# Kernel optimization log

Measured on AMD Instinct MI355X. Metric: run time of the kernel, lower is better.

Reference implementation:

```python
import jax, jax.numpy as jnp
import numpy as np

N_VARS = 4096      # number of discrete variables
CARD = 16          # uniform cardinality per variable
N_HIDDEN = 256
POP = 1024         # pop_size (batch)
N_VISIBLE = N_VARS * CARD  # 65536


def setup_inputs() -> dict:
    key = jax.random.key(0)
    k1, k2, k3 = jax.random.split(key, 3)
    # hidden units are binary stochastic in the RBM; uniform [0,1) works for the math
    hidden = jax.random.uniform(k1, (POP, N_HIDDEN), dtype=jnp.float32)
    W = jax.random.normal(k2, (N_VISIBLE, N_HIDDEN), dtype=jnp.float32) * 0.01
    a = jax.random.normal(k3, (N_VISIBLE,), dtype=jnp.float32) * 0.01
    return {"hidden": hidden, "W": W, "a": a}


def reference(hidden, W, a):
    # prob_visible_given_hidden: activation = hidden @ W^T + a  -> [POP, N_VISIBLE]
    act = jnp.einsum('bh,vh->bv', hidden, W) + a
    # per-variable segmented softmax over each block of CARD visible units
    # (uniform cardinality -> reshape to [POP, N_VARS, CARD] and softmax on last axis)
    prob = jax.nn.softmax(act.reshape(POP, N_VARS, CARD), axis=-1)
    return prob.reshape(POP, N_VISIBLE)
```

## Files before the change

kernel.cpp:

```cpp
#include <hip/hip_runtime.h>
#include <hip/hip_bf16.h>


typedef short  bf16x8 __attribute__((ext_vector_type(8)));
typedef float  f32x4  __attribute__((ext_vector_type(4)));

#define NH    256
#define POP   1024
#define NVIS  65536
#define BM    128
#define BN    128
#define BK    32

__device__ __forceinline__ void gld16(void* lds, const void* g) {
  __builtin_amdgcn_global_load_lds(
      (const __attribute__((address_space(1))) void*)g,
      (__attribute__((address_space(3))) void*)lds,
      16, 0, 0);
}
__device__ __forceinline__ unsigned pack2bf(float lo, float hi) {
  return (__float_as_uint(hi) & 0xffff0000u) | (__float_as_uint(lo) >> 16);
}

__global__ __launch_bounds__(256) void cvt_bf16_kernel(
    const float* __restrict__ src, unsigned short* __restrict__ dst, int n8) {
  int i = blockIdx.x * blockDim.x + threadIdx.x;
  const int stride = gridDim.x * blockDim.x;
  for (; i < n8; i += stride) {
    const float4 f0 = ((const float4*)src)[2 * i];
    const float4 f1 = ((const float4*)src)[2 * i + 1];
    uint4 o;
    o.x = pack2bf(f0.x, f0.y); o.y = pack2bf(f0.z, f0.w);
    o.z = pack2bf(f1.x, f1.y); o.w = pack2bf(f1.z, f1.w);
    ((uint4*)dst)[i] = o;
  }
}

__global__ __launch_bounds__(256) void rbm_gemm_kernel(
    const unsigned short* __restrict__ Wb,
    const unsigned short* __restrict__ Hb,
    const float* __restrict__ Ag,
    float* __restrict__ out)
{
  __shared__ short sA[BM * BK];
  __shared__ short sB[BN * BK];

  const int tid  = threadIdx.x;
  const int lane = tid & 63;
  const int wave = tid >> 6;
  const int wm   = wave & 1;
  const int wn   = wave >> 1;
  const int quad = lane >> 4;
  const int col  = lane & 15;

  const int m_base = blockIdx.y * BM;
  const int n_base = blockIdx.x * BN;

  f32x4 acc[4][4];
  #pragma unroll
  for (int i = 0; i < 4; ++i)
    #pragma unroll
    for (int j = 0; j < 4; ++j)
      acc[i][j] = f32x4{0.f, 0.f, 0.f, 0.f};

  for (int kk = 0; kk < NH / BK; ++kk) {
    const int k0 = kk * BK;
    if (kk) __syncthreads();

    #pragma unroll
    for (int t = 0; t < 2; ++t) {
      const int c   = t * 256 + tid;
      const int row = c >> 2;
      const int cio = (c & 3) * 8;
      gld16(&sA[row * BK + cio], Wb + (size_t)(m_base + row) * NH + k0 + cio);
      gld16(&sB[row * BK + cio], Hb + (size_t)(n_base + row) * NH + k0 + cio);
    }
    __syncthreads();

    bf16x8 af[4], bfr[4];
    #pragma unroll
    for (int mt = 0; mt < 4; ++mt)
      af[mt] = *(const bf16x8*)&sA[(wm * 64 + mt * 16 + col) * BK + quad * 8];
    #pragma unroll
    for (int nt = 0; nt < 4; ++nt)
      bfr[nt] = *(const bf16x8*)&sB[(wn * 64 + nt * 16 + col) * BK + quad * 8];

    #pragma unroll
    for (int mt = 0; mt < 4; ++mt)
      #pragma unroll
      for (int nt = 0; nt < 4; ++nt)
        acc[mt][nt] = __builtin_amdgcn_mfma_f32_16x16x32_bf16(
            af[mt], bfr[nt], acc[mt][nt], 0, 0, 0);
  }

  #pragma unroll
  for (int mt = 0; mt < 4; ++mt) {
    const int v0 = m_base + wm * 64 + mt * 16 + quad * 4;
    const float4 av = *(const float4*)(Ag + v0);
    #pragma unroll
    for (int nt = 0; nt < 4; ++nt) {
      const int b = n_base + wn * 64 + nt * 16 + col;
      f32x4 c = acc[mt][nt];
      float x0 = c[0] + av.x, x1 = c[1] + av.y;
      float x2 = c[2] + av.z, x3 = c[3] + av.w;
      float mx = fmaxf(fmaxf(x0, x1), fmaxf(x2, x3));
      mx = fmaxf(mx, __shfl_xor(mx, 16));
      mx = fmaxf(mx, __shfl_xor(mx, 32));
      float e0 = __expf(x0 - mx), e1 = __expf(x1 - mx);
      float e2 = __expf(x2 - mx), e3 = __expf(x3 - mx);
      float s = (e0 + e1) + (e2 + e3);
      s += __shfl_xor(s, 16);
      s += __shfl_xor(s, 32);
      const float inv = 1.0f / s;
      f32x4 o;
      o[0] = e0 * inv; o[1] = e1 * inv; o[2] = e2 * inv; o[3] = e3 * inv;
      __builtin_nontemporal_store(o, (f32x4*)(out + (size_t)b * NVIS + v0));
    }
  }
}

__global__ __launch_bounds__(256) void rbm_softmax_fb(
    const float* __restrict__ Wg, const float* __restrict__ Hg,
    const float* __restrict__ Ag, float* __restrict__ out)
{
  __shared__ short sA[BM * BK];
  __shared__ short sB[BN * BK];
  const int tid = threadIdx.x, lane = tid & 63, wave = tid >> 6;
  const int wm = wave & 1, wn = wave >> 1, quad = lane >> 4, col = lane & 15;
  const int m_base = blockIdx.y * BM, n_base = blockIdx.x * BN;
  const int r0 = tid >> 3, c0 = (tid & 7) * 4;
  f32x4 acc[4][4];
  #pragma unroll
  for (int i = 0; i < 4; ++i)
    #pragma unroll
    for (int j = 0; j < 4; ++j) acc[i][j] = f32x4{0.f, 0.f, 0.f, 0.f};
  for (int kk = 0; kk < NH / BK; ++kk) {
    const int k0 = kk * BK;
    if (kk) __syncthreads();
    const float* pa = Wg + (size_t)(m_base + r0) * NH + k0 + c0;
    const float* pb = Hg + (size_t)(n_base + r0) * NH + k0 + c0;
    #pragma unroll
    for (int i = 0; i < 4; ++i) {
      const float4 fa = *(const float4*)(pa + (size_t)i * 32 * NH);
      const float4 fb = *(const float4*)(pb + (size_t)i * 32 * NH);
      uint2 ua, ub;
      ua.x = pack2bf(fa.x, fa.y); ua.y = pack2bf(fa.z, fa.w);
      ub.x = pack2bf(fb.x, fb.y); ub.y = pack2bf(fb.z, fb.w);
      *(uint2*)&sA[(i * 32 + r0) * BK + c0] = ua;
      *(uint2*)&sB[(i * 32 + r0) * BK + c0] = ub;
    }
    __syncthreads();
    bf16x8 af[4], bfr[4];
    #pragma unroll
    for (int mt = 0; mt < 4; ++mt)
      af[mt] = *(const bf16x8*)&sA[(wm * 64 + mt * 16 + col) * BK + quad * 8];
    #pragma unroll
    for (int nt = 0; nt < 4; ++nt)
      bfr[nt] = *(const bf16x8*)&sB[(wn * 64 + nt * 16 + col) * BK + quad * 8];
    #pragma unroll
    for (int mt = 0; mt < 4; ++mt)
      #pragma unroll
      for (int nt = 0; nt < 4; ++nt)
        acc[mt][nt] = __builtin_amdgcn_mfma_f32_16x16x32_bf16(
            af[mt], bfr[nt], acc[mt][nt], 0, 0, 0);
  }
  #pragma unroll
  for (int mt = 0; mt < 4; ++mt) {
    const int v0 = m_base + wm * 64 + mt * 16 + quad * 4;
    const float4 av = *(const float4*)(Ag + v0);
    #pragma unroll
    for (int nt = 0; nt < 4; ++nt) {
      const int b = n_base + wn * 64 + nt * 16 + col;
      f32x4 c = acc[mt][nt];
      float x0 = c[0] + av.x, x1 = c[1] + av.y;
      float x2 = c[2] + av.z, x3 = c[3] + av.w;
      float mx = fmaxf(fmaxf(x0, x1), fmaxf(x2, x3));
      mx = fmaxf(mx, __shfl_xor(mx, 16));
      mx = fmaxf(mx, __shfl_xor(mx, 32));
      float e0 = __expf(x0 - mx), e1 = __expf(x1 - mx);
      float e2 = __expf(x2 - mx), e3 = __expf(x3 - mx);
      float s = (e0 + e1) + (e2 + e3);
      s += __shfl_xor(s, 16); s += __shfl_xor(s, 32);
      const float inv = 1.0f / s;
      float4 o;
      o.x = e0 * inv; o.y = e1 * inv; o.z = e2 * inv; o.w = e3 * inv;
      *(float4*)(out + (size_t)b * NVIS + v0) = o;
    }
  }
}

extern "C" void kernel_launch(void* const* d_in, const int* in_sizes, int n_in,
                              void* d_out, int out_size, void* d_ws, size_t ws_size,
                              hipStream_t stream) {
  const float* hidden = (const float*)d_in[0];
  const float* W      = (const float*)d_in[1];
  const float* a      = (const float*)d_in[2];
  float* out          = (float*)d_out;

  const size_t w_elems = (size_t)NVIS * NH;
  const size_t h_elems = (size_t)POP * NH;
  const size_t need = (w_elems + h_elems) * sizeof(unsigned short);

  dim3 grid(POP / BN, NVIS / BM);

  if (ws_size >= need) {
    unsigned short* Wb = (unsigned short*)d_ws;
    unsigned short* Hb = Wb + w_elems;
    cvt_bf16_kernel<<<2048, 256, 0, stream>>>(W, Wb, (int)(w_elems / 8));
    cvt_bf16_kernel<<<128, 256, 0, stream>>>(hidden, Hb, (int)(h_elems / 8));
    rbm_gemm_kernel<<<grid, 256, 0, stream>>>(Wb, Hb, a, out);
  } else {
    rbm_softmax_fb<<<grid, 256, 0, stream>>>(W, hidden, a, out);
  }
}
```

Measured before the change: 394.0 us.

## Fuse bf16 conversion into GEMM, keep hidden tile resident in LDS

Drops the separate fp32-to-bf16 conversion kernels and the workspace round trip. Each block now converts its 128-row hidden tile once into LDS, holding all of K. Each wave streams W rows straight from global memory into registers, converts them in place with a one-step register prefetch, and runs MFMAs against the resident B tile before the fused softmax epilogue. This removes the extra W read/write pass and the per-K-step barriers. In exchange, W fragments are loaded without LDS sharing, and the larger accumulator set (4x8 tiles) raises register pressure under launch bounds of 2 blocks per CU.

```diff
diff --git a/kernel.cpp b/kernel.cpp
--- a/kernel.cpp
+++ b/kernel.cpp
@@ -1,5 +1,4 @@
 #include <hip/hip_runtime.h>
-#include <hip/hip_bf16.h>
 
 
 typedef short  bf16x8 __attribute__((ext_vector_type(8)));
@@ -8,183 +7,128 @@
 #define NH    256
 #define POP   1024
 #define NVIS  65536
-#define BM    128
 #define BN    128
-#define BK    32
+#define MB    1024
+#define SUBM  64
 
-__device__ __forceinline__ void gld16(void* lds, const void* g) {
-  __builtin_amdgcn_global_load_lds(
-      (const __attribute__((address_space(1))) void*)g,
-      (__attribute__((address_space(3))) void*)lds,
-      16, 0, 0);
-}
 __device__ __forceinline__ unsigned pack2bf(float lo, float hi) {
   return (__float_as_uint(hi) & 0xffff0000u) | (__float_as_uint(lo) >> 16);
 }
 
-__global__ __launch_bounds__(256) void cvt_bf16_kernel(
-    const float* __restrict__ src, unsigned short* __restrict__ dst, int n8) {
-  int i = blockIdx.x * blockDim.x + threadIdx.x;
-  const int stride = gridDim.x * blockDim.x;
-  for (; i < n8; i += stride) {
-    const float4 f0 = ((const float4*)src)[2 * i];
-    const float4 f1 = ((const float4*)src)[2 * i + 1];
-    uint4 o;
-    o.x = pack2bf(f0.x, f0.y); o.y = pack2bf(f0.z, f0.w);
-    o.z = pack2bf(f1.x, f1.y); o.w = pack2bf(f1.z, f1.w);
-    ((uint4*)dst)[i] = o;
-  }
-}
-
-__global__ __launch_bounds__(256) void rbm_gemm_kernel(
-    const unsigned short* __restrict__ Wb,
-    const unsigned short* __restrict__ Hb,
+__global__ __launch_bounds__(256, 2) void rbm_fused_kernel(
+    const float* __restrict__ Hg,
+    const float* __restrict__ Wg,
     const float* __restrict__ Ag,
     float* __restrict__ out)
 {
-  __shared__ short sA[BM * BK];
-  __shared__ short sB[BN * BK];
+  __shared__ short sB[8 * BN * 32];
 
   const int tid  = threadIdx.x;
   const int lane = tid & 63;
   const int wave = tid >> 6;
-  const int wm   = wave & 1;
-  const int wn   = wave >> 1;
   const int quad = lane >> 4;
   const int col  = lane & 15;
+  const int n_base = blockIdx.x * BN;
+  const int m_blk  = blockIdx.y * MB;
 
-  const int m_base = blockIdx.y * BM;
-  const int n_base = blockIdx.x * BN;
+  {
+    const int row  = tid >> 1;
+    const int half = (tid & 1) * 16;
+    const float* src = Hg + (size_t)(n_base + row) * NH + half;
+    #pragma unroll
+    for (int j = 0; j < 8; ++j) {
+      const float4 f0 = ((const float4*)(src + j * 32))[0];
+      const float4 f1 = ((const float4*)(src + j * 32))[1];
+      const float4 f2 = ((const float4*)(src + j * 32))[2];
+      const float4 f3 = ((const float4*)(src + j * 32))[3];
+      uint4 u0, u1;
+      u0.x = pack2bf(f0.x, f0.y); u0.y = pack2bf(f0.z, f0.w);
+      u0.z = pack2bf(f1.x, f1.y); u0.w = pack2bf(f1.z, f1.w);
+      u1.x = pack2bf(f2.x, f2.y); u1.y = pack2bf(f2.z, f2.w);
+      u1.z = pack2bf(f3.x, f3.y); u1.w = pack2bf(f3.z, f3.w);
+      *(uint4*)&sB[(j * BN + row) * 32 + half]     = u0;
+      *(uint4*)&sB[(j * BN + row) * 32 + half + 8] = u1;
+    }
+  }
+  __syncthreads();
 
-  f32x4 acc[4][4];
-  #pragma unroll
-  for (int i = 0; i < 4; ++i)
-    #pragma unroll
-    for (int j = 0; j < 4; ++j)
-      acc[i][j] = f32x4{0.f, 0.f, 0.f, 0.f};
+  #pragma unroll 1
+  for (int t = 0; t < MB / (4 * SUBM); ++t) {
+    const int m0 = m_blk + wave * (MB / 4) + t * SUBM;
 
-  for (int kk = 0; kk < NH / BK; ++kk) {
-    const int k0 = kk * BK;
-    if (kk) __syncthreads();
-
-    #pragma unroll
-    for (int t = 0; t < 2; ++t) {
-      const int c   = t * 256 + tid;
-      const int row = c >> 2;
-      const int cio = (c & 3) * 8;
-      gld16(&sA[row * BK + cio], Wb + (size_t)(m_base + row) * NH + k0 + cio);
-      gld16(&sB[row * BK + cio], Hb + (size_t)(n_base + row) * NH + k0 + cio);
-    }
-    __syncthreads();
-
-    bf16x8 af[4], bfr[4];
-    #pragma unroll
-    for (int mt = 0; mt < 4; ++mt)
-      af[mt] = *(const bf16x8*)&sA[(wm * 64 + mt * 16 + col) * BK + quad * 8];
-    #pragma unroll
-    for (int nt = 0; nt < 4; ++nt)
-      bfr[nt] = *(const bf16x8*)&sB[(wn * 64 + nt * 16 + col) * BK + quad * 8];
-
+    f32x4 acc[4][8];
     #pragma unroll
     for (int mt = 0; mt < 4; ++mt)
       #pragma unroll
-      for (int nt = 0; nt < 4; ++nt)
-        acc[mt][nt] = __builtin_amdgcn_mfma_f32_16x16x32_bf16(
-            af[mt], bfr[nt], acc[mt][nt], 0, 0, 0);
-  }
+      for (int nt = 0; nt < 8; ++nt)
+        acc[mt][nt] = f32x4{0.f, 0.f, 0.f, 0.f};
 
-  #pragma unroll
-  for (int mt = 0; mt < 4; ++mt) {
-    const int v0 = m_base + wm * 64 + mt * 16 + quad * 4;
-    const float4 av = *(const float4*)(Ag + v0);
-    #pragma unroll
-    for (int nt = 0; nt < 4; ++nt) {
-      const int b = n_base + wn * 64 + nt * 16 + col;
-      f32x4 c = acc[mt][nt];
-      float x0 = c[0] + av.x, x1 = c[1] + av.y;
-      float x2 = c[2] + av.z, x3 = c[3] + av.w;
-      float mx = fmaxf(fmaxf(x0, x1), fmaxf(x2, x3));
-      mx = fmaxf(mx, __shfl_xor(mx, 16));
-      mx = fmaxf(mx, __shfl_xor(mx, 32));
-      float e0 = __expf(x0 - mx), e1 = __expf(x1 - mx);
-      float e2 = __expf(x2 - mx), e3 = __expf(x3 - mx);
-      float s = (e0 + e1) + (e2 + e3);
-      s += __shfl_xor(s, 16);
-      s += __shfl_xor(s, 32);
-      const float inv = 1.0f / s;
-      f32x4 o;
-      o[0] = e0 * inv; o[1] = e1 * inv; o[2] = e2 * inv; o[3] = e3 * inv;
-      __builtin_nontemporal_store(o, (f32x4*)(out + (size_t)b * NVIS + v0));
-    }
-  }
-}
-
-__global__ __launch_bounds__(256) void rbm_softmax_fb(
-    const float* __restrict__ Wg, const float* __restrict__ Hg,
-    const float* __restrict__ Ag, float* __restrict__ out)
-{
-  __shared__ short sA[BM * BK];
-  __shared__ short sB[BN * BK];
-  const int tid = threadIdx.x, lane = tid & 63, wave = tid >> 6;
-  const int wm = wave & 1, wn = wave >> 1, quad = lane >> 4, col = lane & 15;
-  const int m_base = blockIdx.y * BM, n_base = blockIdx.x * BN;
-  const int r0 = tid >> 3, c0 = (tid & 7) * 4;
-  f32x4 acc[4][4];
-  #pragma unroll
-  for (int i = 0; i < 4; ++i)
-    #pragma unroll
-    for (int j = 0; j < 4; ++j) acc[i][j] = f32x4{0.f, 0.f, 0.f, 0.f};
-  for (int kk = 0; kk < NH / BK; ++kk) {
-    const int k0 = kk * BK;
-    if (kk) __syncthreads();
-    const float* pa = Wg + (size_t)(m_base + r0) * NH + k0 + c0;
-    const float* pb = Hg + (size_t)(n_base + r0) * NH + k0 + c0;
-    #pragma unroll
-    for (int i = 0; i < 4; ++i) {
-      const float4 fa = *(const float4*)(pa + (size_t)i * 32 * NH);
-      const float4 fb = *(const float4*)(pb + (size_t)i * 32 * NH);
-      uint2 ua, ub;
-      ua.x = pack2bf(fa.x, fa.y); ua.y = pack2bf(fa.z, fa.w);
-      ub.x = pack2bf(fb.x, fb.y); ub.y = pack2bf(fb.z, fb.w);
-      *(uint2*)&sA[(i * 32 + r0) * BK + c0] = ua;
-      *(uint2*)&sB[(i * 32 + r0) * BK + c0] = ub;
-    }
-    __syncthreads();
-    bf16x8 af[4], bfr[4];
+    const float* ap[4];
     #pragma unroll
     for (int mt = 0; mt < 4; ++mt)
-      af[mt] = *(const bf16x8*)&sA[(wm * 64 + mt * 16 + col) * BK + quad * 8];
+      ap[mt] = Wg + (size_t)(m0 + mt * 16 + col) * NH + quad * 8;
+
+    float4 pf[4][2];
     #pragma unroll
-    for (int nt = 0; nt < 4; ++nt)
-      bfr[nt] = *(const bf16x8*)&sB[(wn * 64 + nt * 16 + col) * BK + quad * 8];
+    for (int mt = 0; mt < 4; ++mt) {
+      pf[mt][0] = ((const float4*)ap[mt])[0];
+      pf[mt][1] = ((const float4*)ap[mt])[1];
+    }
+
     #pragma unroll
-    for (int mt = 0; mt < 4; ++mt)
+    for (int j = 0; j < 8; ++j) {
+      bf16x8 af[4];
       #pragma unroll
-      for (int nt = 0; nt < 4; ++nt)
-        acc[mt][nt] = __builtin_amdgcn_mfma_f32_16x16x32_bf16(
-            af[mt], bfr[nt], acc[mt][nt], 0, 0, 0);
-  }
-  #pragma unroll
-  for (int mt = 0; mt < 4; ++mt) {
-    const int v0 = m_base + wm * 64 + mt * 16 + quad * 4;
-    const float4 av = *(const float4*)(Ag + v0);
+      for (int mt = 0; mt < 4; ++mt) {
+        union { bf16x8 v; uint4 u; } cv;
+        cv.u.x = pack2bf(pf[mt][0].x, pf[mt][0].y);
+        cv.u.y = pack2bf(pf[mt][0].z, pf[mt][0].w);
+        cv.u.z = pack2bf(pf[mt][1].x, pf[mt][1].y);
+        cv.u.w = pack2bf(pf[mt][1].z, pf[mt][1].w);
+        af[mt] = cv.v;
+      }
+      if (j < 7) {
+        #pragma unroll
+        for (int mt = 0; mt < 4; ++mt) {
+          const float4* p = (const float4*)(ap[mt] + (j + 1) * 32);
+          pf[mt][0] = p[0];
+          pf[mt][1] = p[1];
+        }
+      }
+      const short* bbase = &sB[(j * BN) * 32 + quad * 8];
+      #pragma unroll
+      for (int nt = 0; nt < 8; ++nt) {
+        const bf16x8 bf = *(const bf16x8*)(bbase + (nt * 16 + col) * 32);
+        #pragma unroll
+        for (int mt = 0; mt < 4; ++mt)
+          acc[mt][nt] = __builtin_amdgcn_mfma_f32_16x16x32_bf16(
+              af[mt], bf, acc[mt][nt], 0, 0, 0);
+      }
+    }
+
     #pragma unroll
-    for (int nt = 0; nt < 4; ++nt) {
-      const int b = n_base + wn * 64 + nt * 16 + col;
-      f32x4 c = acc[mt][nt];
-      float x0 = c[0] + av.x, x1 = c[1] + av.y;
-      float x2 = c[2] + av.z, x3 = c[3] + av.w;
-      float mx = fmaxf(fmaxf(x0, x1), fmaxf(x2, x3));
-      mx = fmaxf(mx, __shfl_xor(mx, 16));
-      mx = fmaxf(mx, __shfl_xor(mx, 32));
-      float e0 = __expf(x0 - mx), e1 = __expf(x1 - mx);
-      float e2 = __expf(x2 - mx), e3 = __expf(x3 - mx);
-      float s = (e0 + e1) + (e2 + e3);
-      s += __shfl_xor(s, 16); s += __shfl_xor(s, 32);
-      const float inv = 1.0f / s;
-      float4 o;
-      o.x = e0 * inv; o.y = e1 * inv; o.z = e2 * inv; o.w = e3 * inv;
-      *(float4*)(out + (size_t)b * NVIS + v0) = o;
+    for (int mt = 0; mt < 4; ++mt) {
+      const int v0 = m0 + mt * 16 + quad * 4;
+      const float4 av = *(const float4*)(Ag + v0);
+      #pragma unroll
+      for (int nt = 0; nt < 8; ++nt) {
+        const int b = n_base + nt * 16 + col;
+        f32x4 c = acc[mt][nt];
+        float x0 = c[0] + av.x, x1 = c[1] + av.y;
+        float x2 = c[2] + av.z, x3 = c[3] + av.w;
+        float mx = fmaxf(fmaxf(x0, x1), fmaxf(x2, x3));
+        mx = fmaxf(mx, __shfl_xor(mx, 16));
+        mx = fmaxf(mx, __shfl_xor(mx, 32));
+        float e0 = __expf(x0 - mx), e1 = __expf(x1 - mx);
+        float e2 = __expf(x2 - mx), e3 = __expf(x3 - mx);
+        float s = (e0 + e1) + (e2 + e3);
+        s += __shfl_xor(s, 16);
+        s += __shfl_xor(s, 32);
+        const float inv = 1.0f / s;
+        f32x4 o;
+        o[0] = e0 * inv; o[1] = e1 * inv; o[2] = e2 * inv; o[3] = e3 * inv;
+        __builtin_nontemporal_store(o, (f32x4*)(out + (size_t)b * NVIS + v0));
+      }
     }
   }
 }
@@ -196,20 +140,8 @@
   const float* W      = (const float*)d_in[1];
   const float* a      = (const float*)d_in[2];
   float* out          = (float*)d_out;
+  (void)d_ws; (void)ws_size;
 
-  const size_t w_elems = (size_t)NVIS * NH;
-  const size_t h_elems = (size_t)POP * NH;
-  const size_t need = (w_elems + h_elems) * sizeof(unsigned short);
-
-  dim3 grid(POP / BN, NVIS / BM);
-
-  if (ws_size >= need) {
-    unsigned short* Wb = (unsigned short*)d_ws;
-    unsigned short* Hb = Wb + w_elems;
-    cvt_bf16_kernel<<<2048, 256, 0, stream>>>(W, Wb, (int)(w_elems / 8));
-    cvt_bf16_kernel<<<128, 256, 0, stream>>>(hidden, Hb, (int)(h_elems / 8));
-    rbm_gemm_kernel<<<grid, 256, 0, stream>>>(Wb, Hb, a, out);
-  } else {
-    rbm_softmax_fb<<<grid, 256, 0, stream>>>(W, hidden, a, out);
-  }
+  dim3 grid(POP / BN, NVIS / MB);
+  rbm_fused_kernel<<<grid, 256, 0, stream>>>(hidden, W, a, out);
 }
```

After: 596.7 us. 1.51x slower.
